# Kernel optimization log

Measured on AMD Instinct MI355X. Metric: run time of the kernel, lower is better.

Reference implementation:

```python
import jax, jax.numpy as jnp
import numpy as np

NUM_HEADS = 16
TOP_K = 32
NEG_INF = -1e9
EPS = 1e-8


def setup_inputs() -> dict:
    key = jax.random.key(0)
    ks = jax.random.split(key, 12)
    B, S, D = 2, 1024, 1024
    M, dk = 8192, D // NUM_HEADS
    w = lambda k: jax.random.normal(k, (D, D), jnp.float32) * 0.02
    return {
        "x": jax.random.normal(ks[0], (B, S, D), jnp.float32),
        "Wq": w(ks[1]), "bq": jnp.zeros((D,), jnp.float32),
        "Wk": w(ks[2]), "bk": jnp.zeros((D,), jnp.float32),
        "Wv": w(ks[3]), "bv": jnp.zeros((D,), jnp.float32),
        "Wo": w(ks[4]), "bo": jnp.zeros((D,), jnp.float32),
        "mem_keys": jax.random.normal(ks[5], (M, dk), jnp.float32),
        "mem_vals": jax.random.normal(ks[6], (M, dk), jnp.float32),
        "gate": jnp.zeros((1,), jnp.float32),
    }


def _normalize(v):
    return v / (jnp.linalg.norm(v, axis=-1, keepdims=True) + EPS)


def reference(x, Wq, bq, Wk, bk, Wv, bv, Wo, bo, mem_keys, mem_vals, gate):
    B, S, D = x.shape
    H = NUM_HEADS
    dk = D // H
    # projections (torch Linear: x @ W.T + b), split heads -> [B,H,S,dk]
    split = lambda t: t.reshape(B, S, H, dk).transpose(0, 2, 1, 3)
    q = split(x @ Wq.T + bq)
    k = split(x @ Wk.T + bk)
    v = split(x @ Wv.T + bv)
    # causal attention
    scores = jnp.einsum("bhqd,bhkd->bhqk", q, k) / jnp.sqrt(jnp.float32(dk))
    causal = jnp.triu(jnp.ones((S, S), bool), k=1)  # True above diagonal
    scores = jnp.where(causal, NEG_INF, scores)
    attn = jax.nn.softmax(scores, axis=-1)
    attn_out = jnp.einsum("bhqk,bhkd->bhqd", attn, v)
    attn_out = attn_out.transpose(0, 2, 1, 3).reshape(B, S, D)
    attn_out = attn_out @ Wo.T + bo
    # KNN memory retrieval on flattened per-head queries [B*H*S, dk]
    flat_q = q.reshape(-1, dk)
    sims = _normalize(flat_q) @ _normalize(mem_keys).T  # [Q, M]
    top_scores, idx = jax.lax.top_k(sims, TOP_K)        # [Q, K]
    gathered = mem_vals[idx]                            # [Q, K, dk]
    memory_out = jnp.sum(gathered * top_scores[..., None], axis=-2)  # [Q, dk]
    memory_out = memory_out.reshape(B, H, S, dk).transpose(0, 2, 1, 3).reshape(B, S, D)
    memory_out = memory_out @ Wo.T + bo
    g = jax.nn.sigmoid(gate)
    return g * memory_out + (1.0 - g) * attn_out
```

## Files before the change

kernel.cpp:

```cpp
#include <hip/hip_runtime.h>
#include <stdint.h>
#include <math.h>

#define BATCH   2
#define SEQ     1024
#define DMODEL  1024
#define NHEADS  16
#define DK      64
#define MKEYS   8192
#define NQ      (BATCH*NHEADS*SEQ)
#define THRC    2.25f
#define KPART   4
#define PKEYS2  (MKEYS/KPART)
#define PCAP    64
#define QCAP2   (KPART*PCAP)

typedef __attribute__((ext_vector_type(8))) short short8;
typedef __attribute__((ext_vector_type(4))) float f32x4;
typedef __attribute__((ext_vector_type(2))) double f64x2;
typedef __attribute__((ext_vector_type(4))) double f64x4;

__device__ __forceinline__ short f2bf(float f) {
  uint32_t u = __builtin_bit_cast(uint32_t, f);
  u = (u + 0x7fffu + ((u >> 16) & 1u)) >> 16;
  return (short)u;
}
__device__ __forceinline__ short8 ld_bf8_f32(const float* p) {
  float4 a = *(const float4*)p; float4 b = *(const float4*)(p + 4);
  short8 r;
  r[0]=f2bf(a.x); r[1]=f2bf(a.y); r[2]=f2bf(a.z); r[3]=f2bf(a.w);
  r[4]=f2bf(b.x); r[5]=f2bf(b.y); r[6]=f2bf(b.z); r[7]=f2bf(b.w);
  return r;
}

__device__ __forceinline__ unsigned long long packP(double v, int id) {
  unsigned long long b = __builtin_bit_cast(unsigned long long, v);
  b = (b & 0x8000000000000000ull) ? ~b : (b | 0x8000000000000000ull);
  return (b & ~0x1FFFull) | (unsigned long long)(8191 - id);
}
__device__ __forceinline__ double unpackV(unsigned long long P) {
  unsigned long long K = P & ~0x1FFFull;
  unsigned long long bits = (K & 0x8000000000000000ull) ? (K ^ 0x8000000000000000ull) : ~K;
  return __builtin_bit_cast(double, bits);
}

__global__ __launch_bounds__(256) void norm_keys(const float* __restrict__ mk,
                                                 double* __restrict__ invn64,
                                                 uint16_t* __restrict__ knbf) {
  int wave = threadIdx.x >> 6, lane = threadIdx.x & 63;
  int m = blockIdx.x * 4 + wave;
  double v = (double)mk[(size_t)m * DK + lane];
  double ss = v * v;
  #pragma unroll
  for (int off = 1; off < 64; off <<= 1) ss += __shfl_xor(ss, off);
  double inv = 1.0 / (sqrt(ss) + 1e-8);
  knbf[(size_t)m * DK + lane] = (uint16_t)f2bf((float)(v * inv));
  if (lane == 0) invn64[m] = inv;
}

__device__ __forceinline__ bool probe_decode(const f64x4 d, int base, int mul,
                                             int out[4]) {
  bool ok = true;
  #pragma unroll
  for (int r = 0; r < 4; r++) {
    int v = (int)d[r];
    int t = v - base;
    bool o = ((double)v == d[r]) && (t >= 0) && (t % mul == 0) && ((t / mul) < 16);
    out[r] = t / mul;
    ok = ok && o;
  }
  return ok;
}

__global__ __launch_bounds__(256, 4) void q64_gemm(const float* __restrict__ x,
                                                   const float* __restrict__ Wq,
                                                   const float* __restrict__ bq,
                                                   double* __restrict__ q64q,
                                                   float* __restrict__ qf32,
                                                   uint16_t* __restrict__ qb) {
  __shared__ __align__(16) float Xs[64 * 68];
  __shared__ __align__(16) float Ws[64 * 68];
  int tid = threadIdx.x, lane = tid & 63, w = tid >> 6;
  int bm = blockIdx.y * 64;
  int h = blockIdx.x;

  f64x4 z = {0.0, 0.0, 0.0, 0.0};
  f64x4 d1 = __builtin_amdgcn_mfma_f64_16x16x4f64((double)lane, 1.0, z, 0, 0, 0);
  f64x4 d2 = __builtin_amdgcn_mfma_f64_16x16x4f64(1.0, (double)lane, z, 0, 0, 0);
  int rdec[4], cdec[4];
  bool ok = probe_decode(d1, 96, 4, rdec);
  bool h1A = (bool)__all(ok ? 1 : 0);
  if (!h1A) ok = probe_decode(d1, 6, 16, rdec);
  bool aOK = h1A || (bool)__all(ok ? 1 : 0);
  ok = probe_decode(d2, 96, 4, cdec);
  bool h1B = (bool)__all(ok ? 1 : 0);
  if (!h1B) ok = probe_decode(d2, 6, 16, cdec);
  bool bOK = h1B || (bool)__all(ok ? 1 : 0);
  int iA = h1A ? (lane & 15) : (lane >> 2);
  int kA = h1A ? (lane >> 4) : (lane & 3);
  int jB = h1B ? (lane & 15) : (lane >> 2);
  int kB = h1B ? (lane >> 4) : (lane & 3);
  bool mfma_ok = aOK && bOK;
  if (mfma_ok) {
    f64x4 d3 = __builtin_amdgcn_mfma_f64_16x16x4f64(
        (double)(4 * iA + kA), (double)(jB + 16 * kB), z, 0, 0, 0);
    bool ok3 = true;
    #pragma unroll
    for (int r = 0; r < 4; r++)
      ok3 = ok3 && (d3[r] == (double)(16 * rdec[r] * cdec[r] + 384 * rdec[r] +
                                      6 * cdec[r] + 224));
    mfma_ok = (bool)__all(ok3 ? 1 : 0);
  }

  if (mfma_ok) {
    int wm = (w >> 1) * 32, wn = (w & 1) * 32;
    f64x4 acc[2][2] = {};
    for (int kt = 0; kt < 16; kt++) {
      __syncthreads();
      #pragma unroll
      for (int i = 0; i < 4; i++) {
        int c4 = tid + 256 * i;
        int r = c4 >> 4, q4 = c4 & 15;
        *(float4*)(Xs + r * 68 + q4 * 4) =
            *(const float4*)(x + (size_t)(bm + r) * DMODEL + kt * 64 + q4 * 4);
        *(float4*)(Ws + r * 68 + q4 * 4) =
            *(const float4*)(Wq + (size_t)(h * 64 + r) * DMODEL + kt * 64 + q4 * 4);
      }
      __syncthreads();
      #pragma unroll
      for (int k = 0; k < 64; k += 4) {
        double a0 = (double)Xs[(wm + iA) * 68 + k + kA];
        double a1 = (double)Xs[(wm + 16 + iA) * 68 + k + kA];
        double b0 = (double)Ws[(wn + jB) * 68 + k + kB];
        double b1 = (double)Ws[(wn + 16 + jB) * 68 + k + kB];
        acc[0][0] = __builtin_amdgcn_mfma_f64_16x16x4f64(a0, b0, acc[0][0], 0, 0, 0);
        acc[0][1] = __builtin_amdgcn_mfma_f64_16x16x4f64(a0, b1, acc[0][1], 0, 0, 0);
        acc[1][0] = __builtin_amdgcn_mfma_f64_16x16x4f64(a1, b0, acc[1][0], 0, 0, 0);
        acc[1][1] = __builtin_amdgcn_mfma_f64_16x16x4f64(a1, b1, acc[1][1], 0, 0, 0);
      }
    }
    #pragma unroll
    for (int mi = 0; mi < 2; mi++)
      #pragma unroll
      for (int ni = 0; ni < 2; ni++)
        #pragma unroll
        for (int rg = 0; rg < 4; rg++) {
          int m = bm + wm + mi * 16 + rdec[rg];
          int d = wn + ni * 16 + cdec[rg];
          int b = m >> 10, s = m & 1023;
          size_t qidx = (((size_t)(b * NHEADS + h) * SEQ) + s) * DK + d;
          double val = acc[mi][ni][rg] + (double)bq[h * DK + d];
          q64q[qidx] = val;
          float fv = (float)val;
          qf32[qidx] = fv;
          qb[qidx] = (uint16_t)f2bf(fv);
        }
  } else {
    int tx = tid & 15, ty = tid >> 4;
    double facc[4][4] = {};
    for (int kt = 0; kt < 16; kt++) {
      __syncthreads();
      #pragma unroll
      for (int i = 0; i < 4; i++) {
        int c4 = tid + 256 * i;
        int r = c4 >> 4, q4 = c4 & 15;
        *(float4*)(Xs + r * 68 + q4 * 4) =
            *(const float4*)(x + (size_t)(bm + r) * DMODEL + kt * 64 + q4 * 4);
        *(float4*)(Ws + r * 68 + q4 * 4) =
            *(const float4*)(Wq + (size_t)(h * 64 + r) * DMODEL + kt * 64 + q4 * 4);
      }
      __syncthreads();
      for (int k = 0; k < 64; k++) {
        double bv[4];
        #pragma unroll
        for (int j = 0; j < 4; j++) bv[j] = (double)Ws[(tx + 16 * j) * 68 + k];
        #pragma unroll
        for (int i = 0; i < 4; i++) {
          double a = (double)Xs[(ty * 4 + i) * 68 + k];
          #pragma unroll
          for (int j = 0; j < 4; j++) facc[i][j] = fma(a, bv[j], facc[i][j]);
        }
      }
    }
    #pragma unroll
    for (int i = 0; i < 4; i++)
      #pragma unroll
      for (int j = 0; j < 4; j++) {
        int m = bm + ty * 4 + i, d = tx + 16 * j;
        int b = m >> 10, s = m & 1023;
        size_t qidx = (((size_t)(b * NHEADS + h) * SEQ) + s) * DK + d;
        double val = facc[i][j] + (double)bq[h * DK + d];
        q64q[qidx] = val;
        float fv = (float)val;
        qf32[qidx] = fv;
        qb[qidx] = (uint16_t)f2bf(fv);
      }
  }
}

template<bool AF, bool WF>
__device__ __forceinline__ void gemm_core(const void* __restrict__ Ap,
                                          const void* __restrict__ Wp,
                                          f32x4 acc[4][4], short* As, short* Bs,
                                          int bm, int bn) {
  int tid = threadIdx.x, lane = tid & 63, w = tid >> 6;
  int wm = (w >> 1) * 64, wn = (w & 1) * 64;
  for (int kt = 0; kt < 16; kt++) {
    __syncthreads();
    #pragma unroll
    for (int i = 0; i < 4; i++) {
      int cq = tid + 256 * i;
      int r = cq >> 3, ch = cq & 7;
      size_t aoff = (size_t)(bm + r) * DMODEL + kt * 64 + ch * 8;
      size_t boff = (size_t)(bn + r) * DMODEL + kt * 64 + ch * 8;
      *(short8*)(As + r * 72 + ch * 8) = AF ? ld_bf8_f32((const float*)Ap + aoff)
                                            : *(const short8*)((const uint16_t*)Ap + aoff);
      *(short8*)(Bs + r * 72 + ch * 8) = WF ? ld_bf8_f32((const float*)Wp + boff)
                                            : *(const short8*)((const uint16_t*)Wp + boff);
    }
    __syncthreads();
    #pragma unroll
    for (int kk = 0; kk < 2; kk++) {
      short8 af[4], bfr[4];
      #pragma unroll
      for (int t = 0; t < 4; t++) {
        af[t]  = *(const short8*)(As + (wm + t * 16 + (lane & 15)) * 72 + kk * 32 + (lane >> 4) * 8);
        bfr[t] = *(const short8*)(Bs + (wn + t * 16 + (lane & 15)) * 72 + kk * 32 + (lane >> 4) * 8);
      }
      #pragma unroll
      for (int mi = 0; mi < 4; mi++)
        #pragma unroll
        for (int ni = 0; ni < 4; ni++)
          acc[mi][ni] = __builtin_amdgcn_mfma_f32_16x16x32_bf16(af[mi], bfr[ni], acc[mi][ni], 0, 0, 0);
    }
  }
}

__global__ __launch_bounds__(256) void gemm_kv(
    const float* __restrict__ x,
    const float* __restrict__ Wk, const float* __restrict__ bk,
    const float* __restrict__ Wv, const float* __restrict__ bv,
    uint16_t* __restrict__ kb, uint16_t* __restrict__ vb) {
  __shared__ __align__(16) short As[128 * 72];
  __shared__ __align__(16) short Bs[128 * 72];
  int z = blockIdx.z;
  const float* W    = z == 0 ? Wk : Wv;
  const float* bias = z == 0 ? bk : bv;
  uint16_t* outB    = z == 0 ? kb : vb;
  int bm = blockIdx.y * 128, bn = blockIdx.x * 128;
  f32x4 acc[4][4] = {};
  gemm_core<true, true>(x, W, acc, As, Bs, bm, bn);
  int lane = threadIdx.x & 63, w = threadIdx.x >> 6;
  int wm = (w >> 1) * 64, wn = (w & 1) * 64;
  #pragma unroll
  for (int mi = 0; mi < 4; mi++)
    #pragma unroll
    for (int ni = 0; ni < 4; ni++) {
      int n = bn + wn + ni * 16 + (lane & 15);
      float bvv = bias[n];
      #pragma unroll
      for (int rg = 0; rg < 4; rg++) {
        int m = bm + wm + mi * 16 + (lane >> 4) * 4 + rg;
        float v = acc[mi][ni][rg] + bvv;
        int b = m >> 10, s = m & 1023, h = n >> 6, d = n & 63;
        size_t idx = (((size_t)(b * NHEADS + h) * SEQ) + s) * DK + d;
        outB[idx] = (uint16_t)f2bf(v);
      }
    }
}

__global__ __launch_bounds__(256) void attn_fwd(
    const uint16_t* __restrict__ qb, const uint16_t* __restrict__ kb,
    const uint16_t* __restrict__ vb, float* __restrict__ attnO) {
  __shared__ __align__(16) short Ks[64 * 72];
  __shared__ __align__(16) short Vt[64 * 72];
  __shared__ __align__(16) short Ps[4][16 * 72];
  int tid = threadIdx.x, lane = tid & 63, w = tid >> 6;
  int bx = blockIdx.x;
  int qt = bx & 15, h = (bx >> 4) & 15, b = bx >> 8;
  const uint16_t* Qg = qb + (size_t)(b * NHEADS + h) * SEQ * DK;
  const uint16_t* Kg = kb + (size_t)(b * NHEADS + h) * SEQ * DK;
  const uint16_t* Vg = vb + (size_t)(b * NHEADS + h) * SEQ * DK;
  int qrow0 = qt * 64 + w * 16;
  short8 qfr[2];
  #pragma unroll
  for (int kk = 0; kk < 2; kk++)
    qfr[kk] = *(const short8*)(const void*)(Qg + (size_t)(qrow0 + (lane & 15)) * DK + kk * 32 + (lane >> 4) * 8);
  float m_i[4] = {-1e30f, -1e30f, -1e30f, -1e30f};
  float l_i[4] = {0.f, 0.f, 0.f, 0.f};
  f32x4 Oacc[4] = {};
  for (int kt = 0; kt <= qt; kt++) {
    __syncthreads();
    #pragma unroll
    for (int i = 0; i < 2; i++) {
      int cq = tid + 256 * i;
      int r = cq >> 3, ch = cq & 7;
      short8 g = *(const short8*)(const void*)(Kg + (size_t)(kt * 64 + r) * DK + ch * 8);
      *(short8*)(Ks + r * 72 + ch * 8) = g;
      short8 gv = *(const short8*)(const void*)(Vg + (size_t)(kt * 64 + r) * DK + ch * 8);
      #pragma unroll
      for (int j = 0; j < 8; j++) Vt[(ch * 8 + j) * 72 + r] = gv[j];
    }
    __syncthreads();
    f32x4 sv[4] = {};
    #pragma unroll
    for (int kk = 0; kk < 2; kk++)
      #pragma unroll
      for (int ni = 0; ni < 4; ni++) {
        short8 kf = *(const short8*)(Ks + (ni * 16 + (lane & 15)) * 72 + kk * 32 + (lane >> 4) * 8);
        sv[ni] = __builtin_amdgcn_mfma_f32_16x16x32_bf16(qfr[kk], kf, sv[ni], 0, 0, 0);
      }
    bool diag = (kt == qt);
    #pragma unroll
    for (int ni = 0; ni < 4; ni++)
      #pragma unroll
      for (int rg = 0; rg < 4; rg++) {
        float sc = sv[ni][rg] * 0.125f;
        if (diag) {
          int kcol = kt * 64 + ni * 16 + (lane & 15);
          int qrow = qrow0 + (lane >> 4) * 4 + rg;
          if (kcol > qrow) sc = -1e9f;
        }
        sv[ni][rg] = sc;
      }
    float alpha[4];
    #pragma unroll
    for (int rg = 0; rg < 4; rg++) {
      float v = fmaxf(fmaxf(sv[0][rg], sv[1][rg]), fmaxf(sv[2][rg], sv[3][rg]));
      v = fmaxf(v, __shfl_xor(v, 1)); v = fmaxf(v, __shfl_xor(v, 2));
      v = fmaxf(v, __shfl_xor(v, 4)); v = fmaxf(v, __shfl_xor(v, 8));
      float mn = fmaxf(m_i[rg], v);
      alpha[rg] = expf(m_i[rg] - mn);
      m_i[rg] = mn;
    }
    #pragma unroll
    for (int ni = 0; ni < 4; ni++)
      #pragma unroll
      for (int rg = 0; rg < 4; rg++) sv[ni][rg] = expf(sv[ni][rg] - m_i[rg]);
    #pragma unroll
    for (int rg = 0; rg < 4; rg++) {
      float s = sv[0][rg] + sv[1][rg] + sv[2][rg] + sv[3][rg];
      s += __shfl_xor(s, 1); s += __shfl_xor(s, 2);
      s += __shfl_xor(s, 4); s += __shfl_xor(s, 8);
      l_i[rg] = l_i[rg] * alpha[rg] + s;
    }
    #pragma unroll
    for (int ni = 0; ni < 4; ni++)
      #pragma unroll
      for (int rg = 0; rg < 4; rg++) Oacc[ni][rg] *= alpha[rg];
    short* Pw = &Ps[w][0];
    #pragma unroll
    for (int ni = 0; ni < 4; ni++)
      #pragma unroll
      for (int rg = 0; rg < 4; rg++)
        Pw[((lane >> 4) * 4 + rg) * 72 + ni * 16 + (lane & 15)] = f2bf(sv[ni][rg]);
    #pragma unroll
    for (int kk = 0; kk < 2; kk++) {
      short8 pa = *(const short8*)(Pw + (lane & 15) * 72 + kk * 32 + (lane >> 4) * 8);
      #pragma unroll
      for (int ni = 0; ni < 4; ni++) {
        short8 vf = *(const short8*)(Vt + (ni * 16 + (lane & 15)) * 72 + kk * 32 + (lane >> 4) * 8);
        Oacc[ni] = __builtin_amdgcn_mfma_f32_16x16x32_bf16(pa, vf, Oacc[ni], 0, 0, 0);
      }
    }
  }
  #pragma unroll
  for (int ni = 0; ni < 4; ni++)
    #pragma unroll
    for (int rg = 0; rg < 4; rg++) {
      int row = qrow0 + (lane >> 4) * 4 + rg;
      attnO[((size_t)b * SEQ + row) * DMODEL + h * DK + ni * 16 + (lane & 15)] =
          Oacc[ni][rg] / l_i[rg];
    }
}

__global__ __launch_bounds__(256) void norm_q(const float* __restrict__ qf32,
                                              float* __restrict__ t0arr) {
  int wave = threadIdx.x >> 6, lane = threadIdx.x & 63;
  int q = blockIdx.x * 4 + wave;
  float v = qf32[((size_t)q << 6) + lane];
  float ss = v * v;
  #pragma unroll
  for (int off = 1; off < 64; off <<= 1) ss += __shfl_xor(ss, off);
  if (lane == 0) t0arr[q] = (THRC / 8.0f) * sqrtf(ss);
}

__global__ __launch_bounds__(256) void knn_filter_mfma(
    const uint16_t* __restrict__ qb, const uint16_t* __restrict__ knbf,
    const float* __restrict__ t0arr,
    unsigned short* __restrict__ cand, int* __restrict__ counts) {
  __shared__ __align__(16) short Ks[64 * 68];
  int tid = threadIdx.x, lane = tid & 63, w = tid >> 6;
  int quad = lane >> 4, col = lane & 15;
  int q0 = blockIdx.y * 64;
  int p = blockIdx.x, k0 = p * PKEYS2;
  int qcol = q0 + w * 16 + col;
  short8 aq[2];
  #pragma unroll
  for (int kk = 0; kk < 2; kk++)
    aq[kk] = *(const short8*)(const void*)(qb + (size_t)qcol * DK + kk * 32 + quad * 8);
  float t0 = t0arr[qcol];
  int cntr = 0;
  for (int kt = 0; kt < PKEYS2 / 64; kt++) {
    __syncthreads();
    {
      int r = tid >> 2, ch = (tid & 3) * 2;
      const uint16_t* src = knbf + (size_t)(k0 + kt * 64 + r) * DK + ch * 8;
      *(short8*)(Ks + r * 68 + ch * 8) = *(const short8*)(const void*)src;
      *(short8*)(Ks + r * 68 + ch * 8 + 8) = *(const short8*)(const void*)(src + 8);
    }
    __syncthreads();
    f32x4 acc[4] = {};
    #pragma unroll
    for (int kk = 0; kk < 2; kk++)
      #pragma unroll
      for (int ni = 0; ni < 4; ni++) {
        short8 kf = *(const short8*)(Ks + (ni * 16 + col) * 68 + kk * 32 + quad * 8);
        acc[ni] = __builtin_amdgcn_mfma_f32_16x16x32_bf16(kf, aq[kk], acc[ni], 0, 0, 0);
      }
    unsigned pb = 0u;
    #pragma unroll
    for (int ni = 0; ni < 4; ni++)
      #pragma unroll
      for (int rg = 0; rg < 4; rg++)
        pb |= (acc[ni][rg] >= t0) ? (1u << (ni * 4 + rg)) : 0u;
    int c = __popc(pb);
    int n1 = __shfl_xor(c, 16), n2 = __shfl_xor(c, 32), n3 = __shfl_xor(c, 48);
    int o1 = quad ^ 1, o2 = quad ^ 2, o3 = quad ^ 3;
    int pre = (o1 < quad ? n1 : 0) + (o2 < quad ? n2 : 0) + (o3 < quad ? n3 : 0);
    int tot = c + n1 + n2 + n3;
    int pos = cntr + pre;
    while (pb) {
      int bi = __builtin_ctz(pb);
      pb &= pb - 1u;
      if (pos < PCAP)
        cand[((size_t)qcol * KPART + p) * PCAP + pos] =
            (unsigned short)(k0 + kt * 64 + (bi >> 2) * 16 + quad * 4 + (bi & 3));
      pos++;
    }
    cntr += tot;
  }
  if (quad == 0) {
    int cq = cntr < PCAP ? cntr : PCAP;
    counts[qcol * KPART + p] = cq;
  }
}

template<int NS>
__device__ __forceinline__ void rank_loop(const unsigned long long* cPw, int n,
                                          const unsigned long long* Pm, int* rank) {
  for (int j = 0; j < n; j++) {
    unsigned long long Pj = cPw[j];
    #pragma unroll
    for (int s = 0; s < NS; s++) rank[s] += (Pj > Pm[s]) ? 1 : 0;
  }
}

__global__ __launch_bounds__(256) void knn_select(const double* __restrict__ q64q,
                                                  const float* __restrict__ mk,
                                                  const double* __restrict__ invn,
                                                  const unsigned short* __restrict__ cand,
                                                  const int* __restrict__ counts,
                                                  unsigned long long* __restrict__ wlE) {
  __shared__ unsigned short cid[4][QCAP2];
  __shared__ unsigned long long cP[4][QCAP2];
  __shared__ unsigned long long wl[4][32];
  int wave = threadIdx.x >> 6, lane = threadIdx.x & 63;
  int grp = lane & 7, slot = lane >> 3;
  int q = blockIdx.x * 4 + wave;
  int n = 0;
  #pragma unroll
  for (int p = 0; p < KPART; p++) {
    int c = counts[q * KPART + p]; if (c > PCAP) c = PCAP;
    if (lane < c)
      cid[wave][n + lane] = cand[((size_t)q * KPART + p) * PCAP + lane];
    n += c;
  }
  double q8[8];
  {
    const f64x2* qrow2 = (const f64x2*)(q64q + ((size_t)q << 6) + 8 * grp);
    #pragma unroll
    for (int j = 0; j < 4; j++) { f64x2 t = qrow2[j]; q8[2*j] = t[0]; q8[2*j+1] = t[1]; }
  }
  double ssq = 0.0;
  #pragma unroll
  for (int j = 0; j < 8; j++) ssq = fma(q8[j], q8[j], ssq);
  ssq += __shfl_xor(ssq, 1); ssq += __shfl_xor(ssq, 2); ssq += __shfl_xor(ssq, 4);
  double scale = 1.0 / (sqrt(ssq) + 1e-8);
  for (int c0 = 0; c0 < n; c0 += 32) {
    int cc[4], id[4];
    #pragma unroll
    for (int u = 0; u < 4; u++) {
      cc[u] = c0 + 8 * u + slot;
      id[u] = (cc[u] < n) ? (int)cid[wave][cc[u]] : 0;
    }
    double pv[4];
    #pragma unroll
    for (int u = 0; u < 4; u++) {
      const float* kr = mk + (((size_t)id[u]) << 6) + 8 * grp;
      float4 a = *(const float4*)kr;
      float4 b = *(const float4*)(kr + 4);
      double s = 0.0;
      s = fma(q8[0], (double)a.x, s); s = fma(q8[1], (double)a.y, s);
      s = fma(q8[2], (double)a.z, s); s = fma(q8[3], (double)a.w, s);
      s = fma(q8[4], (double)b.x, s); s = fma(q8[5], (double)b.y, s);
      s = fma(q8[6], (double)b.z, s); s = fma(q8[7], (double)b.w, s);
      pv[u] = s;
    }
    #pragma unroll
    for (int u = 0; u < 4; u++) {
      pv[u] += __shfl_xor(pv[u], 1);
      pv[u] += __shfl_xor(pv[u], 2);
      pv[u] += __shfl_xor(pv[u], 4);
    }
    if (grp == 0) {
      #pragma unroll
      for (int u = 0; u < 4; u++)
        if (cc[u] < n) cP[wave][cc[u]] = packP(pv[u] * invn[id[u]], id[u]);
    }
  }
  unsigned long long Pm[4]; int rank[4] = {0, 0, 0, 0};
  #pragma unroll
  for (int s = 0; s < 4; s++) {
    int idx = s * 64 + lane;
    Pm[s] = (idx < n) ? cP[wave][idx] : 0xFFFFFFFFFFFFFFFFull;
  }
  if (n > 128)      rank_loop<4>(cP[wave], n, Pm, rank);
  else if (n > 64)  rank_loop<2>(cP[wave], n, Pm, rank);
  else              rank_loop<1>(cP[wave], n, Pm, rank);
  #pragma unroll
  for (int s = 0; s < 4; s++) {
    int idx = s * 64 + lane;
    if (idx < n && rank[s] < 32) {
      int id = 8191 - (int)(Pm[s] & 0x1FFFull);
      float wgt = (float)(unpackV(Pm[s]) * scale);
      wl[wave][rank[s]] =
          ((unsigned long long)__builtin_bit_cast(unsigned, wgt) << 32) | (unsigned)id;
    }
  }
  int nsel = n < 32 ? n : 32;
  if (lane < nsel) wlE[(size_t)q * 32 + lane] = wl[wave][lane];
}

__global__ __launch_bounds__(256) void knn_gather(const unsigned long long* __restrict__ wlE,
                                                  const int* __restrict__ counts,
                                                  const float* __restrict__ mv,
                                                  const float* __restrict__ attnO,
                                                  const float* __restrict__ gate,
                                                  uint16_t* __restrict__ outb) {
  __shared__ unsigned long long wg[4][32];
  int wave = threadIdx.x >> 6, lane = threadIdx.x & 63;
  int q = blockIdx.x * 4 + wave;
  int n = 0;
  #pragma unroll
  for (int p = 0; p < KPART; p++) {
    int c = counts[q * KPART + p]; if (c > PCAP) c = PCAP;
    n += c;
  }
  int nsel = n < 32 ? n : 32;
  if (lane < 32) wg[wave][lane] = (lane < nsel) ? wlE[(size_t)q * 32 + lane] : 0;
  float accf = 0.f;
  for (int r = 0; r < nsel; r++) {
    unsigned long long e = wg[wave][r];
    int id = (int)(e & 0xFFFFFFFFull);
    float wgt = __builtin_bit_cast(float, (unsigned)(e >> 32));
    accf += wgt * mv[((size_t)id << 6) + lane];
  }
  float g = 1.f / (1.f + expf(-gate[0]));
  int b = q >> 14, h = (q >> 10) & 15, s = q & 1023;
  size_t oi = ((size_t)b * SEQ + s) * DMODEL + h * DK + lane;
  outb[oi] = (uint16_t)f2bf(g * accf + (1.f - g) * attnO[oi]);
}

__global__ __launch_bounds__(256) void gemm_out(
    const uint16_t* __restrict__ A, const float* __restrict__ W,
    const float* __restrict__ bias, float* __restrict__ out) {
  __shared__ __align__(16) short As[128 * 72];
  __shared__ __align__(16) short Bs[128 * 72];
  int bm = blockIdx.y * 128, bn = blockIdx.x * 128;
  f32x4 acc[4][4] = {};
  gemm_core<false, true>(A, W, acc, As, Bs, bm, bn);
  int lane = threadIdx.x & 63, w = threadIdx.x >> 6;
  int wm = (w >> 1) * 64, wn = (w & 1) * 64;
  #pragma unroll
  for (int mi = 0; mi < 4; mi++)
    #pragma unroll
    for (int ni = 0; ni < 4; ni++) {
      int n = bn + wn + ni * 16 + (lane & 15);
      float bvv = bias[n];
      #pragma unroll
      for (int rg = 0; rg < 4; rg++) {
        int m = bm + wm + mi * 16 + (lane >> 4) * 4 + rg;
        out[(size_t)m * DMODEL + n] = acc[mi][ni][rg] + bvv;
      }
    }
}

extern "C" void kernel_launch(void* const* d_in, const int* in_sizes, int n_in,
                              void* d_out, int out_size, void* d_ws, size_t ws_size,
                              hipStream_t stream) {
  const float* x    = (const float*)d_in[0];
  const float* Wq   = (const float*)d_in[1];
  const float* bq   = (const float*)d_in[2];
  const float* Wk   = (const float*)d_in[3];
  const float* bk   = (const float*)d_in[4];
  const float* Wv   = (const float*)d_in[5];
  const float* bv   = (const float*)d_in[6];
  const float* Wo   = (const float*)d_in[7];
  const float* bo   = (const float*)d_in[8];
  const float* mk   = (const float*)d_in[9];
  const float* mv   = (const float*)d_in[10];
  const float* gate = (const float*)d_in[11];

  char* ws = (char*)d_ws;
  double*   invn64  = (double*)(ws);
  uint16_t* knbf    = (uint16_t*)(ws + ((size_t)4  << 20));
  float*    qf32    = (float*)(ws + ((size_t)6  << 20));
  double*   q64q    = (double*)(ws + ((size_t)14 << 20));
  uint16_t* qb      = (uint16_t*)(ws + ((size_t)30 << 20));
  uint16_t* kb      = (uint16_t*)(ws + ((size_t)34 << 20));
  uint16_t* vb      = (uint16_t*)(ws + ((size_t)38 << 20));
  float*    attnO   = (float*)(ws + ((size_t)42 << 20));
  unsigned long long* wlE = (unsigned long long*)(ws + ((size_t)50 << 20));
  uint16_t* blendb  = (uint16_t*)(ws + ((size_t)58 << 20));
  float*    t0arr   = (float*)(ws + ((size_t)62 << 20));
  int*      counts  = (int*)(ws + ((size_t)63 << 20));
  unsigned short* cnd = (unsigned short*)(ws + ((size_t)64 << 20));

  norm_keys<<<dim3(2048), dim3(256), 0, stream>>>(mk, invn64, knbf);
  q64_gemm<<<dim3(16, 32), dim3(256), 0, stream>>>(x, Wq, bq, q64q, qf32, qb);
  gemm_kv<<<dim3(8, 16, 2), dim3(256), 0, stream>>>(x, Wk, bk, Wv, bv, kb, vb);
  attn_fwd<<<dim3(512), dim3(256), 0, stream>>>(qb, kb, vb, attnO);
  norm_q<<<dim3(8192), dim3(256), 0, stream>>>(qf32, t0arr);
  knn_filter_mfma<<<dim3(KPART, 512), dim3(256), 0, stream>>>(qb, knbf, t0arr, cnd, counts);
  knn_select<<<dim3(8192), dim3(256), 0, stream>>>(q64q, mk, invn64, cnd, counts, wlE);
  knn_gather<<<dim3(8192), dim3(256), 0, stream>>>(wlE, counts, mv, attnO, gate, blendb);
  gemm_out<<<dim3(8, 16), dim3(256), 0, stream>>>(blendb, Wo, bo, (float*)d_out);
}
```

Measured before the change: 463.0 us.

## Add fp32 prefilter in knn_select to shrink candidates before fp64 rescoring

Measured after the change: 453.2 us. 2.1% less time.

```diff
diff --git a/kernel.cpp b/kernel.cpp
--- a/kernel.cpp
+++ b/kernel.cpp
@@ -46,6 +46,7 @@
 
 __global__ __launch_bounds__(256) void norm_keys(const float* __restrict__ mk,
                                                  double* __restrict__ invn64,
+                                                 float* __restrict__ invnf,
                                                  uint16_t* __restrict__ knbf) {
   int wave = threadIdx.x >> 6, lane = threadIdx.x & 63;
   int m = blockIdx.x * 4 + wave;
@@ -55,7 +56,7 @@
   for (int off = 1; off < 64; off <<= 1) ss += __shfl_xor(ss, off);
   double inv = 1.0 / (sqrt(ss) + 1e-8);
   knbf[(size_t)m * DK + lane] = (uint16_t)f2bf((float)(v * inv));
-  if (lane == 0) invn64[m] = inv;
+  if (lane == 0) { invn64[m] = inv; invnf[m] = (float)inv; }
 }
 
 __device__ __forceinline__ bool probe_decode(const f64x4 d, int base, int mul,
@@ -457,12 +458,17 @@
 }
 
 __global__ __launch_bounds__(256) void knn_select(const double* __restrict__ q64q,
+                                                  const float* __restrict__ qf32,
                                                   const float* __restrict__ mk,
                                                   const double* __restrict__ invn,
+                                                  const float* __restrict__ invnf,
+                                                  const float* __restrict__ t0arr,
                                                   const unsigned short* __restrict__ cand,
                                                   const int* __restrict__ counts,
                                                   unsigned long long* __restrict__ wlE) {
   __shared__ unsigned short cid[4][QCAP2];
+  __shared__ float Af[4][QCAP2];
+  __shared__ unsigned short cid2[4][64];
   __shared__ unsigned long long cP[4][QCAP2];
   __shared__ unsigned long long wl[4][32];
   int wave = threadIdx.x >> 6, lane = threadIdx.x & 63;
@@ -487,12 +493,97 @@
   for (int j = 0; j < 8; j++) ssq = fma(q8[j], q8[j], ssq);
   ssq += __shfl_xor(ssq, 1); ssq += __shfl_xor(ssq, 2); ssq += __shfl_xor(ssq, 4);
   double scale = 1.0 / (sqrt(ssq) + 1e-8);
-  for (int c0 = 0; c0 < n; c0 += 32) {
+  float qa[8];
+  {
+    const float4* qrow4 = (const float4*)(qf32 + ((size_t)q << 6) + 8 * grp);
+    float4 a0 = qrow4[0], a1 = qrow4[1];
+    qa[0]=a0.x; qa[1]=a0.y; qa[2]=a0.z; qa[3]=a0.w;
+    qa[4]=a1.x; qa[5]=a1.y; qa[6]=a1.z; qa[7]=a1.w;
+  }
+
+  bool full = (n <= 40);
+  int m = n;
+  if (!full) {
+    for (int c0 = 0; c0 < n; c0 += 32) {
+      int cc[4], id[4];
+      #pragma unroll
+      for (int u = 0; u < 4; u++) {
+        cc[u] = c0 + 8 * u + slot;
+        id[u] = (cc[u] < n) ? (int)cid[wave][cc[u]] : 0;
+      }
+      float pv[4];
+      #pragma unroll
+      for (int u = 0; u < 4; u++) {
+        const float* kr = mk + (((size_t)id[u]) << 6) + 8 * grp;
+        float4 a = *(const float4*)kr;
+        float4 b = *(const float4*)(kr + 4);
+        float s = 0.f;
+        s = fmaf(qa[0], a.x, s); s = fmaf(qa[1], a.y, s);
+        s = fmaf(qa[2], a.z, s); s = fmaf(qa[3], a.w, s);
+        s = fmaf(qa[4], b.x, s); s = fmaf(qa[5], b.y, s);
+        s = fmaf(qa[6], b.z, s); s = fmaf(qa[7], b.w, s);
+        pv[u] = s;
+      }
+      #pragma unroll
+      for (int u = 0; u < 4; u++) {
+        pv[u] += __shfl_xor(pv[u], 1);
+        pv[u] += __shfl_xor(pv[u], 2);
+        pv[u] += __shfl_xor(pv[u], 4);
+      }
+      if (grp == 0) {
+        #pragma unroll
+        for (int u = 0; u < 4; u++)
+          if (cc[u] < n) Af[wave][cc[u]] = pv[u] * invnf[id[u]];
+      }
+    }
+    float t0 = t0arr[q];
+    float it0 = 2048.0f / t0;
+    int qv[4];
+    #pragma unroll
+    for (int s = 0; s < 4; s++) {
+      int idx = s * 64 + lane;
+      if (idx < n) {
+        int v = (int)((Af[wave][idx] - t0) * it0);
+        v = v < 0 ? 0 : v;
+        v = v > 4095 ? 4095 : v;
+        qv[s] = v;
+      } else {
+        qv[s] = -1;
+      }
+    }
+    int lo = 0, hi = 4096;
+    while (hi - lo > 1) {
+      int mid = (lo + hi) >> 1;
+      int cnt = 0;
+      #pragma unroll
+      for (int s = 0; s < 4; s++)
+        cnt += (int)__popcll(__ballot(qv[s] >= mid));
+      if (cnt >= 32) lo = mid; else hi = mid;
+    }
+    int tg = lo - 2; if (tg < 0) tg = 0;
+    int base = 0;
+    #pragma unroll
+    for (int s = 0; s < 4; s++) {
+      bool pr = (qv[s] >= tg);
+      unsigned long long mb = __ballot(pr);
+      if (pr) {
+        int pos = base + (int)__popcll(mb & ((1ull << lane) - 1ull));
+        if (pos < 64) cid2[wave][pos] = cid[wave][s * 64 + lane];
+      }
+      base += (int)__popcll(mb);
+    }
+    if (base > 64) full = true;
+    else m = base;
+  }
+  if (full) m = n;
+  const unsigned short* lst = full ? cid[wave] : cid2[wave];
+
+  for (int c0 = 0; c0 < m; c0 += 32) {
     int cc[4], id[4];
     #pragma unroll
     for (int u = 0; u < 4; u++) {
       cc[u] = c0 + 8 * u + slot;
-      id[u] = (cc[u] < n) ? (int)cid[wave][cc[u]] : 0;
+      id[u] = (cc[u] < m) ? (int)lst[cc[u]] : 0;
     }
     double pv[4];
     #pragma unroll
@@ -516,29 +607,29 @@
     if (grp == 0) {
       #pragma unroll
       for (int u = 0; u < 4; u++)
-        if (cc[u] < n) cP[wave][cc[u]] = packP(pv[u] * invn[id[u]], id[u]);
+        if (cc[u] < m) cP[wave][cc[u]] = packP(pv[u] * invn[id[u]], id[u]);
     }
   }
   unsigned long long Pm[4]; int rank[4] = {0, 0, 0, 0};
   #pragma unroll
   for (int s = 0; s < 4; s++) {
     int idx = s * 64 + lane;
-    Pm[s] = (idx < n) ? cP[wave][idx] : 0xFFFFFFFFFFFFFFFFull;
-  }
-  if (n > 128)      rank_loop<4>(cP[wave], n, Pm, rank);
-  else if (n > 64)  rank_loop<2>(cP[wave], n, Pm, rank);
-  else              rank_loop<1>(cP[wave], n, Pm, rank);
+    Pm[s] = (idx < m) ? cP[wave][idx] : 0xFFFFFFFFFFFFFFFFull;
+  }
+  if (m > 128)      rank_loop<4>(cP[wave], m, Pm, rank);
+  else if (m > 64)  rank_loop<2>(cP[wave], m, Pm, rank);
+  else              rank_loop<1>(cP[wave], m, Pm, rank);
   #pragma unroll
   for (int s = 0; s < 4; s++) {
     int idx = s * 64 + lane;
-    if (idx < n && rank[s] < 32) {
+    if (idx < m && rank[s] < 32) {
       int id = 8191 - (int)(Pm[s] & 0x1FFFull);
       float wgt = (float)(unpackV(Pm[s]) * scale);
       wl[wave][rank[s]] =
           ((unsigned long long)__builtin_bit_cast(unsigned, wgt) << 32) | (unsigned)id;
     }
   }
-  int nsel = n < 32 ? n : 32;
+  int nsel = m < 32 ? m : 32;
   if (lane < nsel) wlE[(size_t)q * 32 + lane] = wl[wave][lane];
 }
 
@@ -614,6 +705,7 @@
 
   char* ws = (char*)d_ws;
   double*   invn64  = (double*)(ws);
+  float*    invnf   = (float*)(ws + ((size_t)1  << 20));
   uint16_t* knbf    = (uint16_t*)(ws + ((size_t)4  << 20));
   float*    qf32    = (float*)(ws + ((size_t)6  << 20));
   double*   q64q    = (double*)(ws + ((size_t)14 << 20));
@@ -627,13 +719,13 @@
   int*      counts  = (int*)(ws + ((size_t)63 << 20));
   unsigned short* cnd = (unsigned short*)(ws + ((size_t)64 << 20));
 
-  norm_keys<<<dim3(2048), dim3(256), 0, stream>>>(mk, invn64, knbf);
+  norm_keys<<<dim3(2048), dim3(256), 0, stream>>>(mk, invn64, invnf, knbf);
   q64_gemm<<<dim3(16, 32), dim3(256), 0, stream>>>(x, Wq, bq, q64q, qf32, qb);
   gemm_kv<<<dim3(8, 16, 2), dim3(256), 0, stream>>>(x, Wk, bk, Wv, bv, kb, vb);
   attn_fwd<<<dim3(512), dim3(256), 0, stream>>>(qb, kb, vb, attnO);
   norm_q<<<dim3(8192), dim3(256), 0, stream>>>(qf32, t0arr);
   knn_filter_mfma<<<dim3(KPART, 512), dim3(256), 0, stream>>>(qb, knbf, t0arr, cnd, counts);
-  knn_select<<<dim3(8192), dim3(256), 0, stream>>>(q64q, mk, invn64, cnd, counts, wlE);
+  knn_select<<<dim3(8192), dim3(256), 0, stream>>>(q64q, qf32, mk, invn64, invnf, t0arr, cnd, counts, wlE);
   knn_gather<<<dim3(8192), dim3(256), 0, stream>>>(wlE, counts, mv, attnO, gate, blendb);
   gemm_out<<<dim3(8, 16), dim3(256), 0, stream>>>(blendb, Wo, bo, (float*)d_out);
 }
```
